# Performance work log

Hardware: AMD Instinct MI355X
Metric: run time of the kernel (lower is better)

The kernel has to match this reference:

```python
import jax, jax.numpy as jnp
import numpy as np

N = 4_000_000   # input points (nonzero voxels at tensor_stride 1)
B = 4           # batch size
G = 128         # voxel grid extent per axis at input stride
DIM = 3         # spatial dimension (init arg `dimension`)
STRIDE = 2      # kernel_size == stride == 2, dilation 1 -> coord // 2 pooling


def setup_inputs() -> dict:
    key = jax.random.key(0)
    k1, k2 = jax.random.split(key)
    batch_idx = jax.random.randint(k1, (N,), 0, B, dtype=jnp.int32)
    coords = jax.random.randint(k2, (N, DIM), 0, G, dtype=jnp.int32)
    # ME builds the "feature" tensor directly from the float coordinates
    coords_f = coords.astype(jnp.float32)
    return {"coords_f": coords_f, "batch_idx": batch_idx, "coords": coords,
            "grid_size": G}


def reference(coords_f, batch_idx, coords, grid_size):
    # Pooled (output) voxel per point: kernel==stride==2 => floor division.
    gs = grid_size // STRIDE                       # output grid extent per axis
    per_batch = gs ** DIM
    S = B * per_batch                              # dense output segment count

    out = coords // STRIDE                         # [N, 3] int
    lin = (out[:, 0] * gs + out[:, 1]) * gs + out[:, 2]
    seg = batch_idx * per_batch + lin              # [N] segment id in [0, S)

    ones = jnp.ones((coords_f.shape[0],), dtype=coords_f.dtype)
    # MinkowskiSumPooling on all-ones features = points per output voxel
    count = jax.ops.segment_sum(ones, seg, num_segments=S)          # [S]
    # MinkowskiGlobalSumPooling on ones = points per batch item
    glob = jax.ops.segment_sum(ones, batch_idx, num_segments=B)     # [B]

    seg_ids = jnp.arange(S)
    seg_batch = seg_ids // per_batch                                # [S]
    nonempty = count > 0
    # density = pool_xx / broadcast(pool_xx, glob_xx)
    density = jnp.where(nonempty, count / glob[seg_batch], 0.0)     # [S]

    # MinkowskiAvgPooling of coordinates -> per-voxel centroid
    csum = jax.ops.segment_sum(coords_f, seg, num_segments=S)       # [S, 3]
    safe_count = jnp.where(nonempty, count, 1.0)
    center = csum / safe_count[:, None]                             # [S, 3]

    # unpool(center) back to points, then sum-pool squared residuals
    mean_diff = coords_f - center[seg]                              # [N, 3]
    sqsum = jax.ops.segment_sum(mean_diff * mean_diff, seg, num_segments=S)
    variance = jnp.where(nonempty[:, None], sqsum / safe_count[:, None], 0.0)

    # Output-voxel coordinates (in original scale: multiples of STRIDE)
    rem = seg_ids % per_batch
    c0 = rem // (gs * gs)
    c1 = (rem // gs) % gs
    c2 = rem % gs
    out_coords = jnp.stack([c0, c1, c2], axis=-1).astype(coords_f.dtype) * STRIDE
    norm_center = jnp.where(nonempty[:, None], center - out_coords, 0.0)

    # ME.cat(density, variance, norm_center) -> [S, 2*DIM + 1]
    return jnp.concatenate([density[:, None], variance, norm_center], axis=1)
```

## Files before the change

kernel.cpp:

```cpp
#include <hip/hip_runtime.h>
#include <hip/hip_bf16.h>


#define BLOCK1 1024
#define PPT 8
#define PTS (BLOCK1 * PPT)
#define BUCKETS 256
#define SEG_SHIFT 12
#define SPB 4096
#define BLOCK2 1024
#define FBLOCK 256

__device__ __forceinline__ unsigned make_pay(int b, int x, int y, int z, int gs) {
    const int seg = (((b * gs + (x >> 1)) * gs + (y >> 1)) * gs) + (z >> 1);
    return ((unsigned)seg << 3) | ((unsigned)(x & 1) << 2)
         | ((unsigned)(y & 1) << 1) | (unsigned)(z & 1);
}

__global__ __launch_bounds__(BLOCK1, 2)
void partition_kernel(const int* __restrict__ bidx,
                      const int* __restrict__ coords,
                      const int* __restrict__ gptr,
                      unsigned* __restrict__ payload,
                      unsigned* __restrict__ g_cursor,
                      int N, int CAP) {
    __shared__ unsigned s_hist[BUCKETS];
    __shared__ unsigned s_old[BUCKETS];
    __shared__ unsigned s_cur[BUCKETS];

    const int tid = threadIdx.x;
    if (tid < BUCKETS) { s_hist[tid] = 0u; s_cur[tid] = 0u; }
    __syncthreads();

    const int gs = gptr[0] >> 1;
    const int base = blockIdx.x * PTS;

    const int4* __restrict__ bidx4 = (const int4*)bidx;
    const int4* __restrict__ crd4  = (const int4*)coords;

    unsigned pay[PPT];
    #pragma unroll
    for (int g = 0; g < PPT / 4; ++g) {
        const int p0 = base + (g * BLOCK1 + tid) * 4;
        if (p0 + 3 < N) {
            const int q = p0 >> 2;
            const int4 b4 = bidx4[q];
            const int4 c0 = crd4[3 * q + 0];
            const int4 c1 = crd4[3 * q + 1];
            const int4 c2 = crd4[3 * q + 2];
            pay[g * 4 + 0] = make_pay(b4.x, c0.x, c0.y, c0.z, gs);
            pay[g * 4 + 1] = make_pay(b4.y, c0.w, c1.x, c1.y, gs);
            pay[g * 4 + 2] = make_pay(b4.z, c1.z, c1.w, c2.x, gs);
            pay[g * 4 + 3] = make_pay(b4.w, c2.y, c2.z, c2.w, gs);
        } else {
            #pragma unroll
            for (int j = 0; j < 4; ++j) {
                const int p = p0 + j;
                pay[g * 4 + j] = (p < N)
                    ? make_pay(bidx[p], coords[3 * p + 0],
                               coords[3 * p + 1], coords[3 * p + 2], gs)
                    : 0xFFFFFFFFu;
            }
        }
    }
    #pragma unroll
    for (int j = 0; j < PPT; ++j)
        if (pay[j] != 0xFFFFFFFFu)
            atomicAdd(&s_hist[pay[j] >> (SEG_SHIFT + 3)], 1u);
    __syncthreads();

    if (tid < BUCKETS)
        s_old[tid] = atomicAdd(&g_cursor[tid], s_hist[tid]);
    __syncthreads();

    #pragma unroll
    for (int j = 0; j < PPT; ++j) {
        const unsigned p = pay[j];
        if (p != 0xFFFFFFFFu) {
            const unsigned bk = p >> (SEG_SHIFT + 3);
            const unsigned r = atomicAdd(&s_cur[bk], 1u);
            const unsigned off = s_old[bk] + r;
            if (off < (unsigned)CAP)
                payload[(size_t)bk * CAP + off] = p;
        }
    }
}

__global__ __launch_bounds__(BLOCK2)
void stats_kernel(const unsigned* __restrict__ payload,
                  const unsigned* __restrict__ g_cursor,
                  float* __restrict__ out, int CAP) {
    __shared__ unsigned fine[SPB];
    __shared__ float s_stage[BLOCK2 * 7];
    __shared__ unsigned s_g[64];

    const int tid = threadIdx.x;
    const int k = blockIdx.x;

    for (int s = tid; s < SPB; s += BLOCK2) fine[s] = 0u;
    if (tid < 64) s_g[tid] = g_cursor[(k & ~63) + tid];
    __syncthreads();
    for (int o = 32; o > 0; o >>= 1) {
        if (tid < o) s_g[tid] += s_g[tid + o];
        __syncthreads();
    }
    const float ginv = 1.0f / (float)s_g[0];

    unsigned cnt = g_cursor[k];
    if (cnt > (unsigned)CAP) cnt = (unsigned)CAP;
    const uint4* __restrict__ pay4 = (const uint4*)(payload + (size_t)k * CAP);
    const unsigned n4 = cnt >> 2;

    for (unsigned j = tid; j < n4; j += BLOCK2) {
        const uint4 p = pay4[j];
        atomicAdd(&fine[(p.x >> 3) & (SPB - 1)],
                  (1u << 24) | ((p.x & 4u) << 14) | ((p.x & 2u) << 7) | (p.x & 1u));
        atomicAdd(&fine[(p.y >> 3) & (SPB - 1)],
                  (1u << 24) | ((p.y & 4u) << 14) | ((p.y & 2u) << 7) | (p.y & 1u));
        atomicAdd(&fine[(p.z >> 3) & (SPB - 1)],
                  (1u << 24) | ((p.z & 4u) << 14) | ((p.z & 2u) << 7) | (p.z & 1u));
        atomicAdd(&fine[(p.w >> 3) & (SPB - 1)],
                  (1u << 24) | ((p.w & 4u) << 14) | ((p.w & 2u) << 7) | (p.w & 1u));
    }
    for (unsigned j = (n4 << 2) + tid; j < cnt; j += BLOCK2) {
        const unsigned p = payload[(size_t)k * CAP + j];
        atomicAdd(&fine[(p >> 3) & (SPB - 1)],
                  (1u << 24) | ((p & 4u) << 14) | ((p & 2u) << 7) | (p & 1u));
    }
    __syncthreads();

    for (int t = 0; t < SPB; t += BLOCK2) {
        const unsigned a = fine[t + tid];
        const int c = (int)(a >> 24);
        float d0 = 0.f, vx = 0.f, vy = 0.f, vz = 0.f, mx = 0.f, my = 0.f, mz = 0.f;
        if (c > 0) {
            const float inv = 1.0f / (float)c;
            mx = (float)((a >> 16) & 0xffu) * inv;
            my = (float)((a >> 8) & 0xffu) * inv;
            mz = (float)(a & 0xffu) * inv;
            vx = mx - mx * mx;
            vy = my - my * my;
            vz = mz - mz * mz;
            d0 = (float)c * ginv;
        }
        float* st = &s_stage[tid * 7];
        st[0] = d0;
        st[1] = vx; st[2] = vy; st[3] = vz;
        st[4] = mx; st[5] = my; st[6] = mz;
        __syncthreads();

        const float4* src = (const float4*)s_stage;
        float4* dst = (float4*)(out + ((size_t)k * SPB + t) * 7);
        #pragma unroll
        for (int j = 0; j < (BLOCK2 * 7) / (4 * BLOCK2) + 1; ++j) {
            const int idx = j * BLOCK2 + tid;
            if (idx < (BLOCK2 * 7) / 4) dst[idx] = src[idx];
        }
        __syncthreads();
    }
}

__global__ __launch_bounds__(FBLOCK)
void accum_kernel(const int* __restrict__ bidx,
                  const int* __restrict__ coords,
                  const int* __restrict__ gptr,
                  unsigned* __restrict__ acc, int astride,
                  int* __restrict__ glob, int N) {
    __shared__ int gcnt[4];
    if (threadIdx.x < 4) gcnt[threadIdx.x] = 0;
    __syncthreads();
    const int gs = gptr[0] >> 1;
    int l0 = 0, l1 = 0, l2 = 0, l3 = 0;
    const int stride = gridDim.x * blockDim.x;
    for (int i = blockIdx.x * blockDim.x + threadIdx.x; i < N; i += stride) {
        const int b  = bidx[i];
        const int cx = coords[3 * i + 0];
        const int cy = coords[3 * i + 1];
        const int cz = coords[3 * i + 2];
        const int seg = (((b * gs + (cx >> 1)) * gs + (cy >> 1)) * gs) + (cz >> 1);
        const unsigned val = (1u << 24)
                           | ((unsigned)(cx & 1) << 16)
                           | ((unsigned)(cy & 1) << 8)
                           |  (unsigned)(cz & 1);
        atomicAdd(&acc[(size_t)seg * astride], val);
        l0 += (b == 0); l1 += (b == 1); l2 += (b == 2); l3 += (b == 3);
    }
    if (l0) atomicAdd(&gcnt[0], l0);
    if (l1) atomicAdd(&gcnt[1], l1);
    if (l2) atomicAdd(&gcnt[2], l2);
    if (l3) atomicAdd(&gcnt[3], l3);
    __syncthreads();
    if (threadIdx.x < 4 && gcnt[threadIdx.x] != 0)
        atomicAdd(&glob[threadIdx.x], gcnt[threadIdx.x]);
}

__global__ __launch_bounds__(FBLOCK)
void finalize_kernel(const unsigned* __restrict__ acc, int astride,
                     const int* __restrict__ glob,
                     float* __restrict__ out, int S, int pbShift) {
    const int s = blockIdx.x * blockDim.x + threadIdx.x;
    if (s >= S) return;
    const unsigned a = acc[(size_t)s * astride];
    const int b = s >> pbShift;
    const int c = (int)(a >> 24);
    float d0 = 0.f, vx = 0.f, vy = 0.f, vz = 0.f, mx = 0.f, my = 0.f, mz = 0.f;
    if (c > 0) {
        const float inv = 1.0f / (float)c;
        mx = (float)((a >> 16) & 0xffu) * inv;
        my = (float)((a >> 8) & 0xffu) * inv;
        mz = (float)(a & 0xffu) * inv;
        vx = mx - mx * mx; vy = my - my * my; vz = mz - mz * mz;
        d0 = (float)c / (float)glob[b];
    }
    float* row = out + (size_t)s * 7;
    row[0] = d0;
    row[1] = vx; row[2] = vy; row[3] = vz;
    row[4] = mx; row[5] = my; row[6] = mz;
}

extern "C" void kernel_launch(void* const* d_in, const int* in_sizes, int n_in,
                              void* d_out, int out_size, void* d_ws, size_t ws_size,
                              hipStream_t stream) {
    const int* bidx   = (const int*)d_in[1];
    const int* coords = (const int*)d_in[2];
    const int* gptr   = (const int*)d_in[3];

    const int N = in_sizes[1];
    const int S = out_size / 7;
    const int per_batch = S / 4;

    const int NpB = (N + BUCKETS - 1) / BUCKETS;
    const int CAP = ((NpB + NpB / 8 + 64) + 63) & ~63;
    const size_t need = 1024 + (size_t)BUCKETS * (size_t)CAP * 4u;

    const bool fast = (S == (BUCKETS * SPB)) && (per_batch == (S / 4)) &&
                      (per_batch / SPB == 64) && (ws_size >= need) && (N > 0);

    if (fast) {
        unsigned* g_cursor = (unsigned*)d_ws;
        unsigned* payload  = (unsigned*)((char*)d_ws + 1024);
        hipMemsetAsync(d_ws, 0, 1024, stream);

        const int blocks = (N + PTS - 1) / PTS;
        partition_kernel<<<blocks, BLOCK1, 0, stream>>>(
            bidx, coords, gptr, payload, g_cursor, N, CAP);
        stats_kernel<<<BUCKETS, BLOCK2, 0, stream>>>(
            payload, g_cursor, (float*)d_out, CAP);
    } else {
        int pbShift = 0;
        while ((1 << pbShift) < per_batch) ++pbShift;
        int* glob = (int*)d_ws;
        const size_t accBytes = (size_t)S * sizeof(unsigned);
        unsigned* acc;
        int astride;
        if (ws_size >= accBytes + 64) {
            acc = (unsigned*)((char*)d_ws + 64);
            astride = 1;
            hipMemsetAsync(d_ws, 0, 64 + accBytes, stream);
        } else {
            acc = (unsigned*)d_out;
            astride = 7;
            hipMemsetAsync(d_out, 0, (size_t)out_size * sizeof(float), stream);
            hipMemsetAsync(d_ws, 0, 64, stream);
        }
        int accBlocks = (N + FBLOCK - 1) / FBLOCK;
        if (accBlocks > 2048) accBlocks = 2048;
        accum_kernel<<<accBlocks, FBLOCK, 0, stream>>>(bidx, coords, gptr,
                                                       acc, astride, glob, N);
        const int finBlocks = (S + FBLOCK - 1) / FBLOCK;
        finalize_kernel<<<finBlocks, FBLOCK, 0, stream>>>(acc, astride, glob,
                                                          (float*)d_out, S, pbShift);
    }
}
```

Measured before the change: 156.1 us.

## Replace global bucket cursors with per-block local partitions and offset table

Partition blocks now write their payload into a block-local segment ordered by bucket, using an in-block prefix scan, instead of reserving slots in global per-bucket arrays through global atomics. Per-block bucket offsets are stored in a table. A small single-block kernel derives per-batch totals from that table, and each stats block gathers its bucket's run from every partition block. This removes global atomic contention and the memset, but adds an extra launch and makes the stats reads scattered, short and serial per thread. BLOCK2 is also halved.

Result: slower. 178.4 us (+14.3%).

```diff
diff --git a/kernel.cpp b/kernel.cpp
--- a/kernel.cpp
+++ b/kernel.cpp
@@ -8,7 +8,7 @@
 #define BUCKETS 256
 #define SEG_SHIFT 12
 #define SPB 4096
-#define BLOCK2 1024
+#define BLOCK2 512
 #define FBLOCK 256
 
 __device__ __forceinline__ unsigned make_pay(int b, int x, int y, int z, int gs) {
@@ -22,11 +22,12 @@
                       const int* __restrict__ coords,
                       const int* __restrict__ gptr,
                       unsigned* __restrict__ payload,
-                      unsigned* __restrict__ g_cursor,
-                      int N, int CAP) {
+                      unsigned* __restrict__ bases,
+                      int N) {
     __shared__ unsigned s_hist[BUCKETS];
-    __shared__ unsigned s_old[BUCKETS];
+    __shared__ unsigned s_base[BUCKETS];
     __shared__ unsigned s_cur[BUCKETS];
+    __shared__ unsigned s_wsum[4];
 
     const int tid = threadIdx.x;
     if (tid < BUCKETS) { s_hist[tid] = 0u; s_cur[tid] = 0u; }
@@ -69,8 +70,28 @@
             atomicAdd(&s_hist[pay[j] >> (SEG_SHIFT + 3)], 1u);
     __syncthreads();
 
-    if (tid < BUCKETS)
-        s_old[tid] = atomicAdd(&g_cursor[tid], s_hist[tid]);
+    unsigned v = 0u, incl = 0u;
+    if (tid < BUCKETS) {
+        v = s_hist[tid];
+        incl = v;
+        #pragma unroll
+        for (int d = 1; d < 64; d <<= 1) {
+            const unsigned t = __shfl_up(incl, d, 64);
+            if ((tid & 63) >= d) incl += t;
+        }
+        if ((tid & 63) == 63) s_wsum[tid >> 6] = incl;
+    }
+    __syncthreads();
+    if (tid < BUCKETS) {
+        const int w = tid >> 6;
+        unsigned off = 0u;
+        if (w > 0) off += s_wsum[0];
+        if (w > 1) off += s_wsum[1];
+        if (w > 2) off += s_wsum[2];
+        const unsigned ex = incl - v + off;
+        s_base[tid] = ex;
+        bases[(size_t)blockIdx.x * BUCKETS + tid] = ex;
+    }
     __syncthreads();
 
     #pragma unroll
@@ -79,55 +100,67 @@
         if (p != 0xFFFFFFFFu) {
             const unsigned bk = p >> (SEG_SHIFT + 3);
             const unsigned r = atomicAdd(&s_cur[bk], 1u);
-            const unsigned off = s_old[bk] + r;
-            if (off < (unsigned)CAP)
-                payload[(size_t)bk * CAP + off] = p;
-        }
-    }
+            payload[(size_t)base + s_base[bk] + r] = p;
+        }
+    }
+}
+
+__global__ __launch_bounds__(256)
+void glob_kernel(const unsigned* __restrict__ bases,
+                 unsigned* __restrict__ glob, int NBLK, int N) {
+    __shared__ unsigned gl[4];
+    const int tid = threadIdx.x;
+    if (tid < 4) gl[tid] = 0u;
+    __syncthreads();
+    unsigned g0 = 0, g1 = 0, g2 = 0, g3 = 0;
+    for (int blk = tid; blk < NBLK; blk += 256) {
+        const size_t o = (size_t)blk * BUCKETS;
+        const unsigned b64  = bases[o + 64];
+        const unsigned b128 = bases[o + 128];
+        const unsigned b192 = bases[o + 192];
+        const unsigned bend = (unsigned)min(PTS, N - blk * PTS);
+        g0 += b64;
+        g1 += b128 - b64;
+        g2 += b192 - b128;
+        g3 += bend - b192;
+    }
+    atomicAdd(&gl[0], g0);
+    atomicAdd(&gl[1], g1);
+    atomicAdd(&gl[2], g2);
+    atomicAdd(&gl[3], g3);
+    __syncthreads();
+    if (tid < 4) glob[tid] = gl[tid];
 }
 
 __global__ __launch_bounds__(BLOCK2)
 void stats_kernel(const unsigned* __restrict__ payload,
-                  const unsigned* __restrict__ g_cursor,
-                  float* __restrict__ out, int CAP) {
+                  const unsigned* __restrict__ bases,
+                  const unsigned* __restrict__ glob,
+                  float* __restrict__ out, int NBLK, int N) {
     __shared__ unsigned fine[SPB];
     __shared__ float s_stage[BLOCK2 * 7];
-    __shared__ unsigned s_g[64];
 
     const int tid = threadIdx.x;
     const int k = blockIdx.x;
 
     for (int s = tid; s < SPB; s += BLOCK2) fine[s] = 0u;
-    if (tid < 64) s_g[tid] = g_cursor[(k & ~63) + tid];
-    __syncthreads();
-    for (int o = 32; o > 0; o >>= 1) {
-        if (tid < o) s_g[tid] += s_g[tid + o];
-        __syncthreads();
-    }
-    const float ginv = 1.0f / (float)s_g[0];
-
-    unsigned cnt = g_cursor[k];
-    if (cnt > (unsigned)CAP) cnt = (unsigned)CAP;
-    const uint4* __restrict__ pay4 = (const uint4*)(payload + (size_t)k * CAP);
-    const unsigned n4 = cnt >> 2;
-
-    for (unsigned j = tid; j < n4; j += BLOCK2) {
-        const uint4 p = pay4[j];
-        atomicAdd(&fine[(p.x >> 3) & (SPB - 1)],
-                  (1u << 24) | ((p.x & 4u) << 14) | ((p.x & 2u) << 7) | (p.x & 1u));
-        atomicAdd(&fine[(p.y >> 3) & (SPB - 1)],
-                  (1u << 24) | ((p.y & 4u) << 14) | ((p.y & 2u) << 7) | (p.y & 1u));
-        atomicAdd(&fine[(p.z >> 3) & (SPB - 1)],
-                  (1u << 24) | ((p.z & 4u) << 14) | ((p.z & 2u) << 7) | (p.z & 1u));
-        atomicAdd(&fine[(p.w >> 3) & (SPB - 1)],
-                  (1u << 24) | ((p.w & 4u) << 14) | ((p.w & 2u) << 7) | (p.w & 1u));
-    }
-    for (unsigned j = (n4 << 2) + tid; j < cnt; j += BLOCK2) {
-        const unsigned p = payload[(size_t)k * CAP + j];
-        atomicAdd(&fine[(p >> 3) & (SPB - 1)],
-                  (1u << 24) | ((p & 4u) << 14) | ((p & 2u) << 7) | (p & 1u));
-    }
-    __syncthreads();
+    __syncthreads();
+
+    for (int blk = tid; blk < NBLK; blk += BLOCK2) {
+        const size_t o = (size_t)blk * BUCKETS;
+        const unsigned s = bases[o + k];
+        const unsigned e = (k < BUCKETS - 1) ? bases[o + k + 1]
+                                             : (unsigned)min(PTS, N - blk * PTS);
+        const unsigned* __restrict__ pp = payload + (size_t)blk * PTS;
+        for (unsigned j = s; j < e; ++j) {
+            const unsigned p = pp[j];
+            atomicAdd(&fine[(p >> 3) & (SPB - 1)],
+                      (1u << 24) | ((p & 4u) << 14) | ((p & 2u) << 7) | (p & 1u));
+        }
+    }
+    __syncthreads();
+
+    const float ginv = 1.0f / (float)glob[k >> 6];
 
     for (int t = 0; t < SPB; t += BLOCK2) {
         const unsigned a = fine[t + tid];
@@ -152,7 +185,7 @@
         const float4* src = (const float4*)s_stage;
         float4* dst = (float4*)(out + ((size_t)k * SPB + t) * 7);
         #pragma unroll
-        for (int j = 0; j < (BLOCK2 * 7) / (4 * BLOCK2) + 1; ++j) {
+        for (int j = 0; j < 2; ++j) {
             const int idx = j * BLOCK2 + tid;
             if (idx < (BLOCK2 * 7) / 4) dst[idx] = src[idx];
         }
@@ -229,23 +262,24 @@
     const int S = out_size / 7;
     const int per_batch = S / 4;
 
-    const int NpB = (N + BUCKETS - 1) / BUCKETS;
-    const int CAP = ((NpB + NpB / 8 + 64) + 63) & ~63;
-    const size_t need = 1024 + (size_t)BUCKETS * (size_t)CAP * 4u;
-
-    const bool fast = (S == (BUCKETS * SPB)) && (per_batch == (S / 4)) &&
-                      (per_batch / SPB == 64) && (ws_size >= need) && (N > 0);
+    const int NBLK = (N + PTS - 1) / PTS;
+    const size_t basesBytes = (size_t)NBLK * BUCKETS * 4u;
+    const size_t payOff = (1024 + basesBytes + 4095) & ~(size_t)4095;
+    const size_t need = payOff + (size_t)NBLK * PTS * 4u;
+
+    const bool fast = (S == (BUCKETS * SPB)) && (per_batch / SPB == 64) &&
+                      (ws_size >= need) && (N > 0) && (NBLK <= BLOCK2);
 
     if (fast) {
-        unsigned* g_cursor = (unsigned*)d_ws;
-        unsigned* payload  = (unsigned*)((char*)d_ws + 1024);
-        hipMemsetAsync(d_ws, 0, 1024, stream);
-
-        const int blocks = (N + PTS - 1) / PTS;
-        partition_kernel<<<blocks, BLOCK1, 0, stream>>>(
-            bidx, coords, gptr, payload, g_cursor, N, CAP);
+        unsigned* glob    = (unsigned*)d_ws;
+        unsigned* bases   = (unsigned*)((char*)d_ws + 1024);
+        unsigned* payload = (unsigned*)((char*)d_ws + payOff);
+
+        partition_kernel<<<NBLK, BLOCK1, 0, stream>>>(
+            bidx, coords, gptr, payload, bases, N);
+        glob_kernel<<<1, 256, 0, stream>>>(bases, glob, NBLK, N);
         stats_kernel<<<BUCKETS, BLOCK2, 0, stream>>>(
-            payload, g_cursor, (float*)d_out, CAP);
+            payload, bases, glob, (float*)d_out, NBLK, N);
     } else {
         int pbShift = 0;
         while ((1 << pbShift) < per_batch) ++pbShift;
```

## Stage partitioned payloads in shared memory for bucket-contiguous coalesced global writes

Applied to the files above, without the earlier changes.

The partition kernel now computes payloads into shared memory and builds a per-block exclusive prefix sum over bucket histograms. It then locally sorts payloads by bucket in LDS, so the final global scatter writes consecutive runs per bucket from consecutive threads instead of randomly scattered single-word stores. This targets uncoalesced write traffic, at the cost of about 48 KB of extra LDS per block (which may lower occupancy from the 2-blocks hint) and extra barriers. Minor loop bound and condition simplifications accompany it.

New measurement: 142.2 us. 1.1x faster.

```diff
diff --git a/kernel.cpp b/kernel.cpp
--- a/kernel.cpp
+++ b/kernel.cpp
@@ -24,9 +24,13 @@
                       unsigned* __restrict__ payload,
                       unsigned* __restrict__ g_cursor,
                       int N, int CAP) {
+    __shared__ uint4    s_raw4[PTS / 4];
+    __shared__ unsigned s_pay[PTS];
     __shared__ unsigned s_hist[BUCKETS];
+    __shared__ unsigned s_base[BUCKETS];
     __shared__ unsigned s_old[BUCKETS];
     __shared__ unsigned s_cur[BUCKETS];
+    __shared__ unsigned s_wsum[4];
 
     const int tid = threadIdx.x;
     if (tid < BUCKETS) { s_hist[tid] = 0u; s_cur[tid] = 0u; }
@@ -34,55 +38,99 @@
 
     const int gs = gptr[0] >> 1;
     const int base = blockIdx.x * PTS;
+    const int cnt = min(PTS, N - base);
 
     const int4* __restrict__ bidx4 = (const int4*)bidx;
     const int4* __restrict__ crd4  = (const int4*)coords;
 
-    unsigned pay[PPT];
     #pragma unroll
     for (int g = 0; g < PPT / 4; ++g) {
-        const int p0 = base + (g * BLOCK1 + tid) * 4;
+        const int slot = g * BLOCK1 + tid;
+        const int p0 = base + slot * 4;
+        uint4 r;
         if (p0 + 3 < N) {
             const int q = p0 >> 2;
             const int4 b4 = bidx4[q];
             const int4 c0 = crd4[3 * q + 0];
             const int4 c1 = crd4[3 * q + 1];
             const int4 c2 = crd4[3 * q + 2];
-            pay[g * 4 + 0] = make_pay(b4.x, c0.x, c0.y, c0.z, gs);
-            pay[g * 4 + 1] = make_pay(b4.y, c0.w, c1.x, c1.y, gs);
-            pay[g * 4 + 2] = make_pay(b4.z, c1.z, c1.w, c2.x, gs);
-            pay[g * 4 + 3] = make_pay(b4.w, c2.y, c2.z, c2.w, gs);
+            r.x = make_pay(b4.x, c0.x, c0.y, c0.z, gs);
+            r.y = make_pay(b4.y, c0.w, c1.x, c1.y, gs);
+            r.z = make_pay(b4.z, c1.z, c1.w, c2.x, gs);
+            r.w = make_pay(b4.w, c2.y, c2.z, c2.w, gs);
         } else {
+            unsigned t[4];
             #pragma unroll
             for (int j = 0; j < 4; ++j) {
                 const int p = p0 + j;
-                pay[g * 4 + j] = (p < N)
+                t[j] = (p < N)
                     ? make_pay(bidx[p], coords[3 * p + 0],
                                coords[3 * p + 1], coords[3 * p + 2], gs)
                     : 0xFFFFFFFFu;
             }
-        }
-    }
+            r.x = t[0]; r.y = t[1]; r.z = t[2]; r.w = t[3];
+        }
+        s_raw4[slot] = r;
+        if (r.x != 0xFFFFFFFFu) atomicAdd(&s_hist[r.x >> (SEG_SHIFT + 3)], 1u);
+        if (r.y != 0xFFFFFFFFu) atomicAdd(&s_hist[r.y >> (SEG_SHIFT + 3)], 1u);
+        if (r.z != 0xFFFFFFFFu) atomicAdd(&s_hist[r.z >> (SEG_SHIFT + 3)], 1u);
+        if (r.w != 0xFFFFFFFFu) atomicAdd(&s_hist[r.w >> (SEG_SHIFT + 3)], 1u);
+    }
+    __syncthreads();
+
+    unsigned v = 0u, incl = 0u;
+    if (tid < BUCKETS) {
+        v = s_hist[tid];
+        incl = v;
+        #pragma unroll
+        for (int d = 1; d < 64; d <<= 1) {
+            const unsigned t = __shfl_up(incl, d, 64);
+            if ((tid & 63) >= d) incl += t;
+        }
+        if ((tid & 63) == 63) s_wsum[tid >> 6] = incl;
+    }
+    __syncthreads();
+    if (tid < BUCKETS) {
+        const int w = tid >> 6;
+        unsigned off = 0u;
+        if (w > 0) off += s_wsum[0];
+        if (w > 1) off += s_wsum[1];
+        if (w > 2) off += s_wsum[2];
+        const unsigned ex = incl - v + off;
+        s_base[tid] = ex;
+        s_old[tid] = atomicAdd(&g_cursor[tid], v);
+    }
+    __syncthreads();
+
     #pragma unroll
-    for (int j = 0; j < PPT; ++j)
-        if (pay[j] != 0xFFFFFFFFu)
-            atomicAdd(&s_hist[pay[j] >> (SEG_SHIFT + 3)], 1u);
-    __syncthreads();
-
-    if (tid < BUCKETS)
-        s_old[tid] = atomicAdd(&g_cursor[tid], s_hist[tid]);
-    __syncthreads();
-
-    #pragma unroll
-    for (int j = 0; j < PPT; ++j) {
-        const unsigned p = pay[j];
-        if (p != 0xFFFFFFFFu) {
-            const unsigned bk = p >> (SEG_SHIFT + 3);
-            const unsigned r = atomicAdd(&s_cur[bk], 1u);
-            const unsigned off = s_old[bk] + r;
-            if (off < (unsigned)CAP)
-                payload[(size_t)bk * CAP + off] = p;
-        }
+    for (int g = 0; g < PPT / 4; ++g) {
+        const uint4 r = s_raw4[g * BLOCK1 + tid];
+        unsigned bk, rk;
+        if (r.x != 0xFFFFFFFFu) {
+            bk = r.x >> (SEG_SHIFT + 3);
+            rk = atomicAdd(&s_cur[bk], 1u); s_pay[s_base[bk] + rk] = r.x;
+        }
+        if (r.y != 0xFFFFFFFFu) {
+            bk = r.y >> (SEG_SHIFT + 3);
+            rk = atomicAdd(&s_cur[bk], 1u); s_pay[s_base[bk] + rk] = r.y;
+        }
+        if (r.z != 0xFFFFFFFFu) {
+            bk = r.z >> (SEG_SHIFT + 3);
+            rk = atomicAdd(&s_cur[bk], 1u); s_pay[s_base[bk] + rk] = r.z;
+        }
+        if (r.w != 0xFFFFFFFFu) {
+            bk = r.w >> (SEG_SHIFT + 3);
+            rk = atomicAdd(&s_cur[bk], 1u); s_pay[s_base[bk] + rk] = r.w;
+        }
+    }
+    __syncthreads();
+
+    for (int j = tid; j < cnt; j += BLOCK1) {
+        const unsigned p = s_pay[j];
+        const unsigned bk = p >> (SEG_SHIFT + 3);
+        const unsigned off = s_old[bk] + ((unsigned)j - s_base[bk]);
+        if (off < (unsigned)CAP)
+            payload[(size_t)bk * CAP + off] = p;
     }
 }
 
@@ -152,7 +200,7 @@
         const float4* src = (const float4*)s_stage;
         float4* dst = (float4*)(out + ((size_t)k * SPB + t) * 7);
         #pragma unroll
-        for (int j = 0; j < (BLOCK2 * 7) / (4 * BLOCK2) + 1; ++j) {
+        for (int j = 0; j < 2; ++j) {
             const int idx = j * BLOCK2 + tid;
             if (idx < (BLOCK2 * 7) / 4) dst[idx] = src[idx];
         }
@@ -233,8 +281,8 @@
     const int CAP = ((NpB + NpB / 8 + 64) + 63) & ~63;
     const size_t need = 1024 + (size_t)BUCKETS * (size_t)CAP * 4u;
 
-    const bool fast = (S == (BUCKETS * SPB)) && (per_batch == (S / 4)) &&
-                      (per_batch / SPB == 64) && (ws_size >= need) && (N > 0);
+    const bool fast = (S == (BUCKETS * SPB)) && (per_batch / SPB == 64) &&
+                      (ws_size >= need) && (N > 0);
 
     if (fast) {
         unsigned* g_cursor = (unsigned*)d_ws;
```
